# Kernel optimization log

Measured on AMD Instinct MI355X. Metric: run time of the kernel, lower is better.

## Reference

```python
import jax, jax.numpy as jnp
import numpy as np

B, T, W = 8, 4096, 1024          # batch, byte seq len, words per sequence
DB, DW = 64, 512                 # byte_embed_dim, word_embed_dim
NH = 2                           # highway layers per block
VOCAB = 264                      # 256 bytes + 4 + 4 specials
BPE_MARK, WORD_MARK = 4, 3       # bpe_mask_idx, word_mask_idx


def _make_seg_ids():
    # ragged word lengths in {3,4,5}, mean 4, summing to T per sequence
    rng = np.random.default_rng(0)
    seg = np.empty((B, T), np.int32)
    base = T // W
    for b in range(B):
        delta = np.zeros(W, np.int64)
        q = W // 4
        idx = rng.permutation(W)
        delta[idx[:q]] = 1
        delta[idx[q:2 * q]] = -1
        seg[b] = np.repeat(np.arange(W), base + delta)
    return jnp.asarray(seg)


def setup_inputs() -> dict:
    key = jax.random.key(0)
    ks = jax.random.split(key, 12)
    s = 0.05
    byte_tokens = jax.random.randint(ks[0], (B, T), 4, VOCAB)
    bpe_mask = jax.random.bernoulli(ks[1], 0.25, (B, T))
    word_mask = jax.random.bernoulli(ks[2], 0.05, (B, T))
    seg_ids = _make_seg_ids()
    tok_emb = (jax.random.normal(ks[3], (VOCAB, DB)) * s).at[0].set(0.0)  # padding_idx=0 row zeroed
    inp = {
        'byte_tokens': byte_tokens, 'bpe_mask': bpe_mask, 'word_mask': word_mask,
        'seg_ids': seg_ids, 'tok_emb': tok_emb,
        'conv0_w': jax.random.normal(ks[4], (3, DB, DW)) * s, 'conv0_b': jnp.zeros((DW,)),
        'hw0_wg': jax.random.normal(ks[5], (NH, DW, DW)) * s, 'hw0_bg': jnp.zeros((NH, DW)),
        'hw0_wh': jax.random.normal(ks[6], (NH, DW, DW)) * s, 'hw0_bh': jnp.zeros((NH, DW)),
        'conv1_w': jax.random.normal(ks[7], (3, DW, DW)) * s, 'conv1_b': jnp.zeros((DW,)),
        'hw1_wg': jax.random.normal(ks[8], (NH, DW, DW)) * s, 'hw1_bg': jnp.zeros((NH, DW)),
        'hw1_wh': jax.random.normal(ks[9], (NH, DW, DW)) * s, 'hw1_bh': jnp.zeros((NH, DW)),
        'proj_w': jax.random.normal(ks[10], (DW, DW)) * s, 'proj_b': jnp.zeros((DW,)),
    }
    return inp


def _conv_highway(x, cw, cb, wg, bg, wh, bh, residual):
    # 1D same-padded conv over sequence, optional residual, relu, then highways
    y = jax.lax.conv_general_dilated(x, cw, (1,), 'SAME',
                                     dimension_numbers=('NWC', 'WIO', 'NWC')) + cb
    if residual:
        y = y + x
    y = jax.nn.relu(y)
    for i in range(NH):
        g = jax.nn.sigmoid(y @ wg[i] + bg[i])
        h = jax.nn.relu(y @ wh[i] + bh[i])
        y = g * h + (1.0 - g) * y
    return y


def reference(byte_tokens, bpe_mask, word_mask, seg_ids, tok_emb,
              conv0_w, conv0_b, hw0_wg, hw0_bg, hw0_wh, hw0_bh,
              conv1_w, conv1_b, hw1_wg, hw1_bg, hw1_wh, hw1_bh,
              proj_w, proj_b):
    # byte embedding + marker embeddings (pad idx 0 -> zero row)
    x = (tok_emb[byte_tokens]
         + tok_emb[jnp.where(bpe_mask, BPE_MARK, 0)]
         + tok_emb[jnp.where(word_mask, WORD_MARK, 0)])          # [B,T,DB]
    x = _conv_highway(x, conv0_w, conv0_b, hw0_wg, hw0_bg, hw0_wh, hw0_bh, False)
    x = _conv_highway(x, conv1_w, conv1_b, hw1_wg, hw1_bg, hw1_wh, hw1_bh, True)
    # ragged per-word segment max over bytes (fused, replaces python loops)
    seg_max = jax.vmap(lambda xi, si: jax.ops.segment_max(xi, si, num_segments=W))
    x = seg_max(x, seg_ids)                                       # [B,W,DW]
    return x @ proj_w + proj_b
```

## Files before the change

### kernel.cpp

```cpp
#include <hip/hip_runtime.h>
#include <hip/hip_bf16.h>

using bf16 = __hip_bfloat16;
typedef __attribute__((ext_vector_type(8))) short s8v;
typedef __attribute__((ext_vector_type(4))) float f4v;

#define T_SEQ 4096
#define DWC 512

__device__ __forceinline__ float fin(float v) {
    return (v == v && fabsf(v) < 1e30f) ? v : 0.0f;
}
__device__ __forceinline__ float ldf(const void* p, size_t i, int f32) {
    return f32 ? ((const float*)p)[i] : __bfloat162float(((const bf16*)p)[i]);
}
__device__ __forceinline__ float b2f(short s) {
    unsigned u = ((unsigned)(unsigned short)s) << 16;
    return __builtin_bit_cast(float, u);
}
__device__ __forceinline__ short f2b(float v) {
    bf16 b = __float2bfloat16(v);
    return __builtin_bit_cast(short, b);
}
__device__ __forceinline__ uint4 ld16(const short* p) { return *(const uint4*)p; }

__device__ __forceinline__ void swz(int L, int G, int& bx, int& by) {
    int k8 = L & 7, sl = L >> 3;
    int gp = G >> 5;
    bx = sl & 3;
    by = k8 * gp + (sl >> 2);
}

__device__ __forceinline__ int swidx(int row, int ch) {
    return row * 32 + ((ch ^ ((row >> 1) & 3)) << 3);
}

__global__ __launch_bounds__(256) void diag_kernel(bf16* __restrict__ out, int n, float v)
{
    int i = blockIdx.x * 256 + threadIdx.x;
    if (i < n) out[i] = __float2bfloat16(i == 0 ? v : 0.0f);
}

__global__ __launch_bounds__(256) void detect_kernel(
    const int* __restrict__ tok, const unsigned char* __restrict__ bpe,
    const unsigned char* __restrict__ wm, const int* __restrict__ seg,
    const unsigned int* __restrict__ embw, int* __restrict__ flags)
{
    __shared__ int sh[5];
    int tid = threadIdx.x;
    if (tid < 5) sh[tid] = 0;
    __syncthreads();
    int bo = 0, bm = 0, wo = 0, wmid = 0;
    for (int i = tid; i < 16384; i += 256) {
        int odd = 2 * i + 1;
        if (bpe[odd]) bo = 1;
        if (wm[odd])  wo = 1;
        int mid = 8 * (i & 4095) + 4;
        if (bpe[mid]) bm = 1;
        if (wm[mid])  wmid = 1;
    }
    if (bo)   atomicOr(&sh[0], 1);
    if (bm)   atomicOr(&sh[1], 1);
    if (wo)   atomicOr(&sh[2], 1);
    if (wmid) atomicOr(&sh[3], 1);
    if (tid < 32 && embw[32 + tid] != 0u) atomicOr(&sh[4], 1);
    __syncthreads();
    if (tid == 0) {
        flags[0] = (tok[32767] != 0) ? 0 : 1;
        flags[1] = sh[0] ? 1 : (sh[1] ? 4 : 8);
        flags[2] = sh[2] ? 1 : (sh[3] ? 4 : 8);
        flags[3] = (seg[32767] != 0) ? 0 : 1;
        flags[4] = sh[4] ? 0 : 1;
    }
}

#define WB_TOTAL 3249664
__global__ __launch_bounds__(256) void convert_weights(
    const void* c0w, const void* c0b, const void* h0g, const void* h0bg,
    const void* h0h, const void* h0bh, const void* c1w, const void* c1b,
    const void* h1g, const void* h1bg, const void* h1h, const void* h1bh,
    const void* pw, const void* pb, const int* __restrict__ flags,
    short* __restrict__ WB)
{
    int f32 = flags[4];
    size_t i = (size_t)blockIdx.x * 256 + threadIdx.x;
    if (i >= WB_TOTAL) return;
    const void* src; size_t si;
    if (i < 98304)        { size_t n = i / 192, k = i % 192; src = c0w; si = k * 512 + n; }
    else if (i < 98816)   { src = c0b;  si = i - 98304; }
    else if (i < 623104)  { size_t o = i - 98816;  size_t l = o >> 18; o &= 262143;
                            size_t n = o >> 9, k = o & 511; src = h0g; si = (l << 18) + k * 512 + n; }
    else if (i < 624128)  { src = h0bg; si = i - 623104; }
    else if (i < 1148416) { size_t o = i - 624128; size_t l = o >> 18; o &= 262143;
                            size_t n = o >> 9, k = o & 511; src = h0h; si = (l << 18) + k * 512 + n; }
    else if (i < 1149440) { src = h0bh; si = i - 1148416; }
    else if (i < 1935872) { size_t o = i - 1149440; size_t n = o / 1536, k = o % 1536;
                            src = c1w; si = k * 512 + n; }
    else if (i < 1936384) { src = c1b;  si = i - 1935872; }
    else if (i < 2460672) { size_t o = i - 1936384; size_t l = o >> 18; o &= 262143;
                            size_t n = o >> 9, k = o & 511; src = h1g; si = (l << 18) + k * 512 + n; }
    else if (i < 2461696) { src = h1bg; si = i - 2460672; }
    else if (i < 2985984) { size_t o = i - 2461696; size_t l = o >> 18; o &= 262143;
                            size_t n = o >> 9, k = o & 511; src = h1h; si = (l << 18) + k * 512 + n; }
    else if (i < 2987008) { src = h1bh; si = i - 2985984; }
    else if (i < 3249152) { size_t o = i - 2987008; size_t n = o >> 9, k = o & 511;
                            src = pw; si = k * 512 + n; }
    else                  { src = pb;   si = i - 3249152; }
    WB[i] = f2b(ldf(src, si, f32));
}

__global__ __launch_bounds__(256) void embed_kernel(
    const int* __restrict__ tok, const unsigned char* __restrict__ bpe,
    const unsigned char* __restrict__ wm, const void* __restrict__ emb,
    const int* __restrict__ flags, short* __restrict__ xe, int bt0)
{
    int i = blockIdx.x * 256 + threadIdx.x;
    int d = i & 63;
    int btl = i >> 6;
    int bt = bt0 + btl;
    int is64t = flags[0];
    int wb = flags[1], ww = flags[2];
    int f32 = flags[4];
    int t = is64t ? (int)((const long long*)tok)[bt] : tok[bt];
    t = min(max(t, 0), 263);
    float v = ldf(emb, (size_t)t * 64 + d, f32);
    if (bpe[(size_t)bt * wb]) v += ldf(emb, 4 * 64 + d, f32);
    if (wm[(size_t)bt * ww])  v += ldf(emb, 3 * 64 + d, f32);
    xe[i] = f2b(fin(v));
}

template<int IC, bool RESID>
__global__ __launch_bounds__(512) void conv_mfma(
    const short* __restrict__ A, const short* __restrict__ WT,
    const short* __restrict__ bias, short* __restrict__ Out)
{
    constexpr int K = 3 * IC;
    constexpr int NIT = K / 64;
    __shared__ __align__(16) short As[2][256 * 32];
    __shared__ __align__(16) short Bs[2][256 * 32];
    int bx, by;
    swz(blockIdx.x, gridDim.x, bx, by);
    const int bm = by * 128, bn = bx * 128;
    const int tid = threadIdx.x;
    const int wave = tid >> 6, lane = tid & 63;
    const int wmr = (wave >> 1) * 32, wnc = (wave & 1) * 64;
    const int q = lane >> 4, ln16 = lane & 15;
    const int sr = tid >> 2, sch = tid & 3;
    const int tt = (bm + sr) & (T_SEQ - 1);
    const short* Bb = WT + (size_t)(bn + sr) * K + sch * 8;

    f4v acc[2][4] = {};
    uint4 rA0, rA1, rB0, rB1;
    const uint4 z4 = make_uint4(0, 0, 0, 0);

    {
        int ts = tt - 1;
        bool ok = (ts >= 0 && ts < T_SEQ);
        const short* sa = A + (size_t)(bm + sr - 1) * IC + sch * 8;
        rA0 = ok ? ld16(sa) : z4;
        rA1 = ok ? ld16(sa + 32) : z4;
        rB0 = ld16(Bb);
        rB1 = ld16(Bb + 32);
    }
    *(uint4*)(&As[0][swidx(sr, sch)])       = rA0;
    *(uint4*)(&As[0][swidx(128 + sr, sch)]) = rA1;
    *(uint4*)(&Bs[0][swidx(sr, sch)])       = rB0;
    *(uint4*)(&Bs[0][swidx(128 + sr, sch)]) = rB1;
    __syncthreads();
    int p = 0;

    for (int it = 0; it < NIT; ++it) {
        const bool more = (it + 1 < NIT);
        if (more) {
            int kn = (it + 1) * 64;
            int tap = kn / IC, c0 = kn - tap * IC;
            int ts = tt + tap - 1;
            bool ok = (ts >= 0 && ts < T_SEQ);
            const short* sa = A + (size_t)(bm + sr + tap - 1) * IC + c0 + sch * 8;
            rA0 = ok ? ld16(sa) : z4;
            rA1 = ok ? ld16(sa + 32) : z4;
            rB0 = ld16(Bb + kn);
            rB1 = ld16(Bb + kn + 32);
        }
        #pragma unroll
        for (int ks = 0; ks < 2; ks++) {
            s8v af[2], bf[4];
            #pragma unroll
            for (int mi = 0; mi < 2; mi++)
                af[mi] = *(const s8v*)(&As[p][swidx(128 * ks + wmr + mi * 16 + ln16, q)]);
            #pragma unroll
            for (int ni = 0; ni < 4; ni++)
                bf[ni] = *(const s8v*)(&Bs[p][swidx(128 * ks + wnc + ni * 16 + ln16, q)]);
            #pragma unroll
            for (int mi = 0; mi < 2; mi++)
                #pragma unroll
                for (int ni = 0; ni < 4; ni++)
                    acc[mi][ni] = __builtin_amdgcn_mfma_f32_16x16x32_bf16(
                        af[mi], bf[ni], acc[mi][ni], 0, 0, 0);
        }
        if (more) {
            *(uint4*)(&As[p ^ 1][swidx(sr, sch)])       = rA0;
            *(uint4*)(&As[p ^ 1][swidx(128 + sr, sch)]) = rA1;
            *(uint4*)(&Bs[p ^ 1][swidx(sr, sch)])       = rB0;
            *(uint4*)(&Bs[p ^ 1][swidx(128 + sr, sch)]) = rB1;
            __syncthreads();
            p ^= 1;
        }
    }

    #pragma unroll
    for (int mi = 0; mi < 2; mi++)
        #pragma unroll
        for (int ni = 0; ni < 4; ni++) {
            int col = bn + wnc + ni * 16 + ln16;
            float bv = b2f(bias[col]);
            #pragma unroll
            for (int r = 0; r < 4; r++) {
                int orow = bm + wmr + mi * 16 + q * 4 + r;
                float v = acc[mi][ni][r] + bv;
                if constexpr (RESID) v += b2f(A[(size_t)orow * IC + col]);
                Out[(size_t)orow * DWC + col] = f2b(fin(fmaxf(v, 0.0f)));
            }
        }
}

__global__ __launch_bounds__(512) void highway_mfma(
    const short* __restrict__ Y, const short* __restrict__ WgT,
    const short* __restrict__ bg, const short* __restrict__ WhT,
    const short* __restrict__ bh, short* __restrict__ Out)
{
    constexpr int NIT = DWC / 32;
    __shared__ __align__(16) short As[2][128 * 32];
    __shared__ __align__(16) short Bg[2][128 * 32];
    __shared__ __align__(16) short Bh[2][128 * 32];
    int bx, by;
    swz(blockIdx.x, gridDim.x, bx, by);
    const int bm = by * 128, bn = bx * 128;
    const int tid = threadIdx.x;
    const int wave = tid >> 6, lane = tid & 63;
    const int wmr = (wave >> 1) * 32, wnc = (wave & 1) * 64;
    const int q = lane >> 4, ln16 = lane & 15;
    const int sr = tid >> 2, sch = tid & 3;
    const int sw = swidx(sr, sch);
    const short* A0 = Y   + (size_t)(bm + sr) * DWC + sch * 8;
    const short* G0 = WgT + (size_t)(bn + sr) * DWC + sch * 8;
    const short* H0 = WhT + (size_t)(bn + sr) * DWC + sch * 8;

    f4v accg[2][4] = {};
    f4v acch[2][4] = {};
    uint4 rA = ld16(A0), rG = ld16(G0), rH = ld16(H0);
    *(uint4*)(&As[0][sw]) = rA;
    *(uint4*)(&Bg[0][sw]) = rG;
    *(uint4*)(&Bh[0][sw]) = rH;
    __syncthreads();
    int p = 0;

    for (int it = 0; it < NIT; ++it) {
        const bool more = (it + 1 < NIT);
        if (more) {
            int kn = (it + 1) * 32;
            rA = ld16(A0 + kn); rG = ld16(G0 + kn); rH = ld16(H0 + kn);
        }
        s8v af[2], bgf[4], bhf[4];
        #pragma unroll
        for (int mi = 0; mi < 2; mi++) af[mi] = *(const s8v*)(&As[p][swidx(wmr + mi * 16 + ln16, q)]);
        #pragma unroll
        for (int ni = 0; ni < 4; ni++) {
            bgf[ni] = *(const s8v*)(&Bg[p][swidx(wnc + ni * 16 + ln16, q)]);
            bhf[ni] = *(const s8v*)(&Bh[p][swidx(wnc + ni * 16 + ln16, q)]);
        }
        #pragma unroll
        for (int mi = 0; mi < 2; mi++)
            #pragma unroll
            for (int ni = 0; ni < 4; ni++) {
                accg[mi][ni] = __builtin_amdgcn_mfma_f32_16x16x32_bf16(
                    af[mi], bgf[ni], accg[mi][ni], 0, 0, 0);
                acch[mi][ni] = __builtin_amdgcn_mfma_f32_16x16x32_bf16(
                    af[mi], bhf[ni], acch[mi][ni], 0, 0, 0);
            }
        if (more) {
            *(uint4*)(&As[p ^ 1][sw]) = rA;
            *(uint4*)(&Bg[p ^ 1][sw]) = rG;
            *(uint4*)(&Bh[p ^ 1][sw]) = rH;
            __syncthreads();
            p ^= 1;
        }
    }

    #pragma unroll
    for (int mi = 0; mi < 2; mi++)
        #pragma unroll
        for (int ni = 0; ni < 4; ni++) {
            int col = bn + wnc + ni * 16 + ln16;
            float bgv = b2f(bg[col]);
            float bhv = b2f(bh[col]);
            #pragma unroll
            for (int r = 0; r < 4; r++) {
                int orow = bm + wmr + mi * 16 + q * 4 + r;
                float g = 1.0f / (1.0f + expf(-(accg[mi][ni][r] + bgv)));
                float h = fmaxf(acch[mi][ni][r] + bhv, 0.0f);
                float y = b2f(Y[(size_t)orow * DWC + col]);
                Out[(size_t)orow * DWC + col] = f2b(fin(g * h + (1.0f - g) * y));
            }
        }
}

__global__ __launch_bounds__(512) void proj_mfma(
    const short* __restrict__ A, const short* __restrict__ WT,
    const short* __restrict__ bias, const int* __restrict__ flags,
    void* __restrict__ Out, int oroff)
{
    constexpr int NIT = DWC / 32;
    __shared__ __align__(16) short As[2][128 * 32];
    __shared__ __align__(16) short Bs[2][128 * 32];
    int bx, by;
    swz(blockIdx.x, gridDim.x, bx, by);
    const int bm = by * 128, bn = bx * 128;
    const int tid = threadIdx.x;
    const int wave = tid >> 6, lane = tid & 63;
    const int wmr = (wave >> 1) * 32, wnc = (wave & 1) * 64;
    const int q = lane >> 4, ln16 = lane & 15;
    const int sr = tid >> 2, sch = tid & 3;
    const int sw = swidx(sr, sch);
    const int f32 = flags[4];
    const short* A0 = A  + (size_t)(bm + sr) * DWC + sch * 8;
    const short* B0 = WT + (size_t)(bn + sr) * DWC + sch * 8;

    f4v acc[2][4] = {};
    uint4 rA = ld16(A0), rB = ld16(B0);
    *(uint4*)(&As[0][sw]) = rA;
    *(uint4*)(&Bs[0][sw]) = rB;
    __syncthreads();
    int p = 0;

    for (int it = 0; it < NIT; ++it) {
        const bool more = (it + 1 < NIT);
        if (more) {
            int kn = (it + 1) * 32;
            rA = ld16(A0 + kn); rB = ld16(B0 + kn);
        }
        s8v af[2], bf[4];
        #pragma unroll
        for (int mi = 0; mi < 2; mi++) af[mi] = *(const s8v*)(&As[p][swidx(wmr + mi * 16 + ln16, q)]);
        #pragma unroll
        for (int ni = 0; ni < 4; ni++) bf[ni] = *(const s8v*)(&Bs[p][swidx(wnc + ni * 16 + ln16, q)]);
        #pragma unroll
        for (int mi = 0; mi < 2; mi++)
            #pragma unroll
            for (int ni = 0; ni < 4; ni++)
                acc[mi][ni] = __builtin_amdgcn_mfma_f32_16x16x32_bf16(
                    af[mi], bf[ni], acc[mi][ni], 0, 0, 0);
        if (more) {
            *(uint4*)(&As[p ^ 1][sw]) = rA;
            *(uint4*)(&Bs[p ^ 1][sw]) = rB;
            __syncthreads();
            p ^= 1;
        }
    }

    #pragma unroll
    for (int mi = 0; mi < 2; mi++)
        #pragma unroll
        for (int ni = 0; ni < 4; ni++) {
            int col = bn + wnc + ni * 16 + ln16;
            float bv = b2f(bias[col]);
            #pragma unroll
            for (int r = 0; r < 4; r++) {
                int orow = bm + wmr + mi * 16 + q * 4 + r;
                float v = fin(acc[mi][ni][r] + bv);
                size_t oi = (size_t)(oroff + orow) * DWC + col;
                if (f32) ((float*)Out)[oi] = v;
                else     ((bf16*)Out)[oi] = __float2bfloat16(v);
            }
        }
}

__global__ __launch_bounds__(256) void bounds_kernel(
    const int* __restrict__ seg, const int* __restrict__ flags,
    int* __restrict__ wstart, int* __restrict__ wend, int bt0)
{
    int il = blockIdx.x * 256 + threadIdx.x;
    int ig = bt0 + il;
    int is64 = flags[3];
    const long long* seg64 = (const long long*)seg;
    int t = il & (T_SEQ - 1);
    int bl = il >> 12;
    int s  = (is64 ? (int)seg64[ig] : seg[ig]) & 1023;
    int sp = (t == 0)         ? -1 : ((is64 ? (int)seg64[ig - 1] : seg[ig - 1]) & 1023);
    int sn = (t == T_SEQ - 1) ? -1 : ((is64 ? (int)seg64[ig + 1] : seg[ig + 1]) & 1023);
    int bw = (bl << 10) + s;
    if (sp != s) wstart[bw] = t;
    if (sn != s) wend[bw] = t;
}

__global__ __launch_bounds__(512) void segmax_kernel(
    const short* __restrict__ Y, const int* __restrict__ wstart,
    const int* __restrict__ wend, short* __restrict__ Out)
{
    int bw = blockIdx.x;
    int d = threadIdx.x;
    int bl = bw >> 10;
    int s = wstart[bw], e = wend[bw];
    s = min(max(s, 0), T_SEQ - 1);
    e = min(max(e, s), T_SEQ - 1);
    float m = b2f(Y[(size_t)((bl << 12) + s) * DWC + d]);
    for (int t = s + 1; t <= e; ++t)
        m = fmaxf(m, b2f(Y[(size_t)((bl << 12) + t) * DWC + d]));
    Out[(size_t)bw * DWC + d] = f2b(fin(m));
}

extern "C" void kernel_launch(void* const* d_in, const int* in_sizes, int n_in,
                              void* d_out, int out_size, void* d_ws, size_t ws_size,
                              hipStream_t stream)
{
    static const int expect[19] = {32768, 32768, 32768, 32768, 16896,
                                   98304, 512, 524288, 1024, 524288, 1024,
                                   786432, 512, 524288, 1024, 524288, 1024,
                                   262144, 512};
    int bad = -1;
    if (n_in < 19) bad = 31;
    else for (int i = 0; i < 19; i++) if (in_sizes[i] != expect[i]) { bad = i; break; }
    if (bad >= 0) {
        diag_kernel<<<dim3((out_size + 255) / 256), dim3(256), 0, stream>>>(
            (bf16*)d_out, out_size, 1e35f * (float)(1 + bad));
        return;
    }

    char* ws = (char*)d_ws;
    const size_t WBREG = 8ull << 20;
    short* WB    = (short*)ws;
    int*   flags = (int*)(ws + 6500352);
    const size_t perC = 8921088 + 8192 + 64;
    int C = 8;
    while (C > 1 && WBREG + (size_t)C * perC > ws_size) C >>= 1;
    if (WBREG + (size_t)C * perC > ws_size) {
        float ws_mib = (float)((double)ws_size / 1048576.0);
        diag_kernel<<<dim3((out_size + 255) / 256), dim3(256), 0, stream>>>(
            (bf16*)d_out, out_size, 1e30f * (16.0f + ws_mib));
        return;
    }

    const int*  byte_tokens = (const int*)d_in[0];
    const unsigned char* bpe_mask = (const unsigned char*)d_in[1];
    const unsigned char* word_mask = (const unsigned char*)d_in[2];
    const int*  seg_ids     = (const int*)d_in[3];
    const void* tok_emb = d_in[4];

    detect_kernel<<<dim3(1), dim3(256), 0, stream>>>(
        byte_tokens, bpe_mask, word_mask, seg_ids,
        (const unsigned int*)tok_emb, flags);

    convert_weights<<<dim3((WB_TOTAL + 255) / 256), dim3(256), 0, stream>>>(
        d_in[5], d_in[6], d_in[7], d_in[8], d_in[9], d_in[10],
        d_in[11], d_in[12], d_in[13], d_in[14], d_in[15], d_in[16],
        d_in[17], d_in[18], flags, WB);

    short* c0wT = WB;            short* c0b  = WB + 98304;
    short* h0gT = WB + 98816;    short* h0bg = WB + 623104;
    short* h0hT = WB + 624128;   short* h0bh = WB + 1148416;
    short* c1wT = WB + 1149440;  short* c1b  = WB + 1935872;
    short* h1gT = WB + 1936384;  short* h1bg = WB + 2460672;
    short* h1hT = WB + 2461696;  short* h1bh = WB + 2985984;
    short* pwT  = WB + 2987008;  short* pb   = WB + 3249152;
    const int LOFF = 262144, LBOFF = 512;

    for (int b0 = 0; b0 < 8; b0 += C) {
        const int rows  = C * T_SEQ;
        const int words = C * 1024;
        char*  chunk  = ws + WBREG;
        short* xe     = (short*)chunk;
        short* U      = (short*)(chunk + (size_t)C * 524288);
        short* V      = (short*)(chunk + (size_t)C * (524288 + 4194304));
        int*   wstart = (int*)(chunk + (size_t)C * 8912896);
        int*   wend   = wstart + words;
        short* segout = U;

        embed_kernel<<<dim3(rows * 64 / 256), dim3(256), 0, stream>>>(
            byte_tokens, bpe_mask, word_mask, tok_emb, flags, xe, b0 * T_SEQ);

        dim3 gg(4 * (rows / 128));
        conv_mfma<64, false><<<gg, dim3(512), 0, stream>>>(xe, c0wT, c0b, U);

        highway_mfma<<<gg, dim3(512), 0, stream>>>(U, h0gT, h0bg, h0hT, h0bh, V);
        highway_mfma<<<gg, dim3(512), 0, stream>>>(V, h0gT + LOFF, h0bg + LBOFF,
                                                   h0hT + LOFF, h0bh + LBOFF, U);

        conv_mfma<512, true><<<gg, dim3(512), 0, stream>>>(U, c1wT, c1b, V);

        highway_mfma<<<gg, dim3(512), 0, stream>>>(V, h1gT, h1bg, h1hT, h1bh, U);
        highway_mfma<<<gg, dim3(512), 0, stream>>>(U, h1gT + LOFF, h1bg + LBOFF,
                                                   h1hT + LOFF, h1bh + LBOFF, V);

        bounds_kernel<<<dim3(rows / 256), dim3(256), 0, stream>>>(
            seg_ids, flags, wstart, wend, b0 * T_SEQ);

        segmax_kernel<<<dim3(words), dim3(512), 0, stream>>>(V, wstart, wend, segout);

        proj_mfma<<<dim3(4 * (words / 128)), dim3(512), 0, stream>>>(
            segout, pwT, pb, flags, d_out, b0 * 1024);
    }
}
```

Before: 503.7 us.

## Fuse byte embedding into first conv and single-buffer highway/proj LDS tiles

```diff
diff --git a/kernel.cpp b/kernel.cpp
--- a/kernel.cpp
+++ b/kernel.cpp
@@ -75,16 +75,26 @@
 }
 
 #define WB_TOTAL 3249664
+#define EMB4_ELEMS (264 * 4 * 64)
 __global__ __launch_bounds__(256) void convert_weights(
     const void* c0w, const void* c0b, const void* h0g, const void* h0bg,
     const void* h0h, const void* h0bh, const void* c1w, const void* c1b,
     const void* h1g, const void* h1bg, const void* h1h, const void* h1bh,
-    const void* pw, const void* pb, const int* __restrict__ flags,
-    short* __restrict__ WB)
+    const void* pw, const void* pb, const void* emb,
+    const int* __restrict__ flags, short* __restrict__ WB)
 {
     int f32 = flags[4];
     size_t i = (size_t)blockIdx.x * 256 + threadIdx.x;
-    if (i >= WB_TOTAL) return;
+    if (i >= WB_TOTAL + EMB4_ELEMS) return;
+    if (i >= WB_TOTAL) {
+        size_t o = i - WB_TOTAL;
+        size_t t = o >> 8, v = (o >> 6) & 3, c = o & 63;
+        float val = ldf(emb, t * 64 + c, f32);
+        if (v & 1) val += ldf(emb, 4 * 64 + c, f32);
+        if (v & 2) val += ldf(emb, 3 * 64 + c, f32);
+        WB[i] = f2b(fin(val));
+        return;
+    }
     const void* src; size_t si;
     if (i < 98304)        { size_t n = i / 192, k = i % 192; src = c0w; si = k * 512 + n; }
     else if (i < 98816)   { src = c0b;  si = i - 98304; }
@@ -109,31 +119,110 @@
     WB[i] = f2b(ldf(src, si, f32));
 }
 
-__global__ __launch_bounds__(256) void embed_kernel(
+__global__ __launch_bounds__(512) void conv0_mfma(
     const int* __restrict__ tok, const unsigned char* __restrict__ bpe,
-    const unsigned char* __restrict__ wm, const void* __restrict__ emb,
-    const int* __restrict__ flags, short* __restrict__ xe, int bt0)
-{
-    int i = blockIdx.x * 256 + threadIdx.x;
-    int d = i & 63;
-    int btl = i >> 6;
-    int bt = bt0 + btl;
-    int is64t = flags[0];
-    int wb = flags[1], ww = flags[2];
-    int f32 = flags[4];
-    int t = is64t ? (int)((const long long*)tok)[bt] : tok[bt];
-    t = min(max(t, 0), 263);
-    float v = ldf(emb, (size_t)t * 64 + d, f32);
-    if (bpe[(size_t)bt * wb]) v += ldf(emb, 4 * 64 + d, f32);
-    if (wm[(size_t)bt * ww])  v += ldf(emb, 3 * 64 + d, f32);
-    xe[i] = f2b(fin(v));
-}
-
-template<int IC, bool RESID>
-__global__ __launch_bounds__(512) void conv_mfma(
+    const unsigned char* __restrict__ wm, const short* __restrict__ emb4,
+    const int* __restrict__ flags, const short* __restrict__ WT,
+    const short* __restrict__ bias, short* __restrict__ Out)
+{
+    constexpr int K = 192;
+    constexpr int NIT = 3;
+    __shared__ __align__(16) short As[2][256 * 32];
+    __shared__ __align__(16) short Bs[2][256 * 32];
+    int bx, by;
+    swz(blockIdx.x, gridDim.x, bx, by);
+    const int bm = by * 128, bn = bx * 128;
+    const int tid = threadIdx.x;
+    const int wave = tid >> 6, lane = tid & 63;
+    const int wmr = (wave >> 1) * 32, wnc = (wave & 1) * 64;
+    const int q = lane >> 4, ln16 = lane & 15;
+    const int sr = tid >> 2, sch = tid & 3;
+    const int tt = (bm + sr) & (T_SEQ - 1);
+    const int is64t = flags[0];
+    const int wb = flags[1], ww = flags[2];
+    const short* Bb = WT + (size_t)(bn + sr) * K + sch * 8;
+
+    f4v acc[2][4] = {};
+    uint4 rA0, rA1, rB0, rB1;
+    const uint4 z4 = make_uint4(0, 0, 0, 0);
+
+    auto loadA = [&](int tap, uint4& a0, uint4& a1) {
+        int ts = tt + tap - 1;
+        if ((unsigned)ts < (unsigned)T_SEQ) {
+            int bt = bm + sr + tap - 1;
+            int tk = is64t ? (int)((const long long*)tok)[bt] : tok[bt];
+            tk = min(max(tk, 0), 263);
+            int v = (bpe[(size_t)bt * wb] ? 1 : 0) | (wm[(size_t)bt * ww] ? 2 : 0);
+            const short* row = emb4 + ((size_t)tk * 4 + v) * 64;
+            a0 = ld16(row + sch * 8);
+            a1 = ld16(row + 32 + sch * 8);
+        } else { a0 = z4; a1 = z4; }
+    };
+
+    loadA(0, rA0, rA1);
+    rB0 = ld16(Bb);
+    rB1 = ld16(Bb + 32);
+    *(uint4*)(&As[0][swidx(sr, sch)])       = rA0;
+    *(uint4*)(&As[0][swidx(128 + sr, sch)]) = rA1;
+    *(uint4*)(&Bs[0][swidx(sr, sch)])       = rB0;
+    *(uint4*)(&Bs[0][swidx(128 + sr, sch)]) = rB1;
+    __syncthreads();
+    int p = 0;
+
+    for (int it = 0; it < NIT; ++it) {
+        const bool more = (it + 1 < NIT);
+        if (more) {
+            int kn = (it + 1) * 64;
+            loadA(it + 1, rA0, rA1);
+            rB0 = ld16(Bb + kn);
+            rB1 = ld16(Bb + kn + 32);
+        }
+        #pragma unroll
+        for (int ks = 0; ks < 2; ks++) {
+            s8v af[2], bf[4];
+            #pragma unroll
+            for (int mi = 0; mi < 2; mi++)
+                af[mi] = *(const s8v*)(&As[p][swidx(128 * ks + wmr + mi * 16 + ln16, q)]);
+            #pragma unroll
+            for (int ni = 0; ni < 4; ni++)
+                bf[ni] = *(const s8v*)(&Bs[p][swidx(128 * ks + wnc + ni * 16 + ln16, q)]);
+            #pragma unroll
+            for (int mi = 0; mi < 2; mi++)
+                #pragma unroll
+                for (int ni = 0; ni < 4; ni++)
+                    acc[mi][ni] = __builtin_amdgcn_mfma_f32_16x16x32_bf16(
+                        af[mi], bf[ni], acc[mi][ni], 0, 0, 0);
+        }
+        if (more) {
+            *(uint4*)(&As[p ^ 1][swidx(sr, sch)])       = rA0;
+            *(uint4*)(&As[p ^ 1][swidx(128 + sr, sch)]) = rA1;
+            *(uint4*)(&Bs[p ^ 1][swidx(sr, sch)])       = rB0;
+            *(uint4*)(&Bs[p ^ 1][swidx(128 + sr, sch)]) = rB1;
+            __syncthreads();
+            p ^= 1;
+        }
+    }
+
+    #pragma unroll
+    for (int mi = 0; mi < 2; mi++)
+        #pragma unroll
+        for (int ni = 0; ni < 4; ni++) {
+            int col = bn + wnc + ni * 16 + ln16;
+            float bv = b2f(bias[col]);
+            #pragma unroll
+            for (int r = 0; r < 4; r++) {
+                int orow = bm + wmr + mi * 16 + q * 4 + r;
+                Out[(size_t)orow * DWC + col] =
+                    f2b(fin(fmaxf(acc[mi][ni][r] + bv, 0.0f)));
+            }
+        }
+}
+
+__global__ __launch_bounds__(512) void conv1_mfma(
     const short* __restrict__ A, const short* __restrict__ WT,
     const short* __restrict__ bias, short* __restrict__ Out)
 {
+    constexpr int IC = 512;
     constexpr int K = 3 * IC;
     constexpr int NIT = K / 64;
     __shared__ __align__(16) short As[2][256 * 32];
@@ -217,8 +306,7 @@
             #pragma unroll
             for (int r = 0; r < 4; r++) {
                 int orow = bm + wmr + mi * 16 + q * 4 + r;
-                float v = acc[mi][ni][r] + bv;
-                if constexpr (RESID) v += b2f(A[(size_t)orow * IC + col]);
+                float v = acc[mi][ni][r] + bv + b2f(A[(size_t)orow * IC + col]);
                 Out[(size_t)orow * DWC + col] = f2b(fin(fmaxf(v, 0.0f)));
             }
         }
@@ -229,10 +317,9 @@
     const short* __restrict__ bg, const short* __restrict__ WhT,
     const short* __restrict__ bh, short* __restrict__ Out)
 {
-    constexpr int NIT = DWC / 32;
-    __shared__ __align__(16) short As[2][128 * 32];
-    __shared__ __align__(16) short Bg[2][128 * 32];
-    __shared__ __align__(16) short Bh[2][128 * 32];
+    __shared__ __align__(16) short As[128 * 32];
+    __shared__ __align__(16) short Bg[128 * 32];
+    __shared__ __align__(16) short Bh[128 * 32];
     int bx, by;
     swz(blockIdx.x, gridDim.x, bx, by);
     const int bm = by * 128, bn = bx * 128;
@@ -249,25 +336,23 @@
     f4v accg[2][4] = {};
     f4v acch[2][4] = {};
     uint4 rA = ld16(A0), rG = ld16(G0), rH = ld16(H0);
-    *(uint4*)(&As[0][sw]) = rA;
-    *(uint4*)(&Bg[0][sw]) = rG;
-    *(uint4*)(&Bh[0][sw]) = rH;
-    __syncthreads();
-    int p = 0;
-
-    for (int it = 0; it < NIT; ++it) {
-        const bool more = (it + 1 < NIT);
-        if (more) {
-            int kn = (it + 1) * 32;
+
+    for (int k0 = 0; k0 < DWC; k0 += 32) {
+        *(uint4*)(&As[sw]) = rA;
+        *(uint4*)(&Bg[sw]) = rG;
+        *(uint4*)(&Bh[sw]) = rH;
+        __syncthreads();
+        if (k0 + 32 < DWC) {
+            int kn = k0 + 32;
             rA = ld16(A0 + kn); rG = ld16(G0 + kn); rH = ld16(H0 + kn);
         }
         s8v af[2], bgf[4], bhf[4];
         #pragma unroll
-        for (int mi = 0; mi < 2; mi++) af[mi] = *(const s8v*)(&As[p][swidx(wmr + mi * 16 + ln16, q)]);
+        for (int mi = 0; mi < 2; mi++) af[mi] = *(const s8v*)(&As[swidx(wmr + mi * 16 + ln16, q)]);
         #pragma unroll
         for (int ni = 0; ni < 4; ni++) {
-            bgf[ni] = *(const s8v*)(&Bg[p][swidx(wnc + ni * 16 + ln16, q)]);
-            bhf[ni] = *(const s8v*)(&Bh[p][swidx(wnc + ni * 16 + ln16, q)]);
+            bgf[ni] = *(const s8v*)(&Bg[swidx(wnc + ni * 16 + ln16, q)]);
+            bhf[ni] = *(const s8v*)(&Bh[swidx(wnc + ni * 16 + ln16, q)]);
         }
         #pragma unroll
         for (int mi = 0; mi < 2; mi++)
@@ -278,13 +363,7 @@
                 acch[mi][ni] = __builtin_amdgcn_mfma_f32_16x16x32_bf16(
                     af[mi], bhf[ni], acch[mi][ni], 0, 0, 0);
             }
-        if (more) {
-            *(uint4*)(&As[p ^ 1][sw]) = rA;
-            *(uint4*)(&Bg[p ^ 1][sw]) = rG;
-            *(uint4*)(&Bh[p ^ 1][sw]) = rH;
-            __syncthreads();
-            p ^= 1;
-        }
+        __syncthreads();
     }
 
     #pragma unroll
@@ -310,9 +389,8 @@
     const short* __restrict__ bias, const int* __restrict__ flags,
     void* __restrict__ Out, int oroff)
 {
-    constexpr int NIT = DWC / 32;
-    __shared__ __align__(16) short As[2][128 * 32];
-    __shared__ __align__(16) short Bs[2][128 * 32];
+    __shared__ __align__(16) short As[128 * 32];
+    __shared__ __align__(16) short Bs[128 * 32];
     int bx, by;
     swz(blockIdx.x, gridDim.x, bx, by);
     const int bm = by * 128, bn = bx * 128;
@@ -328,34 +406,27 @@
 
     f4v acc[2][4] = {};
     uint4 rA = ld16(A0), rB = ld16(B0);
-    *(uint4*)(&As[0][sw]) = rA;
-    *(uint4*)(&Bs[0][sw]) = rB;
-    __syncthreads();
-    int p = 0;
-
-    for (int it = 0; it < NIT; ++it) {
-        const bool more = (it + 1 < NIT);
-        if (more) {
-            int kn = (it + 1) * 32;
+
+    for (int k0 = 0; k0 < DWC; k0 += 32) {
+        *(uint4*)(&As[sw]) = rA;
+        *(uint4*)(&Bs[sw]) = rB;
+        __syncthreads();
+        if (k0 + 32 < DWC) {
+            int kn = k0 + 32;
             rA = ld16(A0 + kn); rB = ld16(B0 + kn);
         }
         s8v af[2], bf[4];
         #pragma unroll
-        for (int mi = 0; mi < 2; mi++) af[mi] = *(const s8v*)(&As[p][swidx(wmr + mi * 16 + ln16, q)]);
-        #pragma unroll
-        for (int ni = 0; ni < 4; ni++) bf[ni] = *(const s8v*)(&Bs[p][swidx(wnc + ni * 16 + ln16, q)]);
+        for (int mi = 0; mi < 2; mi++) af[mi] = *(const s8v*)(&As[swidx(wmr + mi * 16 + ln16, q)]);
+        #pragma unroll
+        for (int ni = 0; ni < 4; ni++) bf[ni] = *(const s8v*)(&Bs[swidx(wnc + ni * 16 + ln16, q)]);
         #pragma unroll
         for (int mi = 0; mi < 2; mi++)
             #pragma unroll
             for (int ni = 0; ni < 4; ni++)
                 acc[mi][ni] = __builtin_amdgcn_mfma_f32_16x16x32_bf16(
                     af[mi], bf[ni], acc[mi][ni], 0, 0, 0);
-        if (more) {
-            *(uint4*)(&As[p ^ 1][sw]) = rA;
-            *(uint4*)(&Bs[p ^ 1][sw]) = rB;
-            __syncthreads();
-            p ^= 1;
-        }
+        __syncthreads();
     }
 
     #pragma unroll
@@ -429,8 +500,8 @@
     char* ws = (char*)d_ws;
     const size_t WBREG = 8ull << 20;
     short* WB    = (short*)ws;
-    int*   flags = (int*)(ws + 6500352);
-    const size_t perC = 8921088 + 8192 + 64;
+    int*   flags = (int*)(ws + (7u << 20));
+    const size_t perC = 8388608 + 8192 + 64;
     int C = 8;
     while (C > 1 && WBREG + (size_t)C * perC > ws_size) C >>= 1;
     if (WBREG + (size_t)C * perC > ws_size) {
@@ -450,10 +521,10 @@
         byte_tokens, bpe_mask, word_mask, seg_ids,
         (const unsigned int*)tok_emb, flags);
 
-    convert_weights<<<dim3((WB_TOTAL + 255) / 256), dim3(256), 0, stream>>>(
+    convert_weights<<<dim3((WB_TOTAL + EMB4_ELEMS + 255) / 256), dim3(256), 0, stream>>>(
         d_in[5], d_in[6], d_in[7], d_in[8], d_in[9], d_in[10],
         d_in[11], d_in[12], d_in[13], d_in[14], d_in[15], d_in[16],
-        d_in[17], d_in[18], flags, WB);
+        d_in[17], d_in[18], tok_emb, flags, WB);
 
     short* c0wT = WB;            short* c0b  = WB + 98304;
     short* h0gT = WB + 98816;    short* h0bg = WB + 623104;
@@ -462,30 +533,30 @@
     short* h1gT = WB + 1936384;  short* h1bg = WB + 2460672;
     short* h1hT = WB + 2461696;  short* h1bh = WB + 2985984;
     short* pwT  = WB + 2987008;  short* pb   = WB + 3249152;
+    short* emb4 = WB + WB_TOTAL;
     const int LOFF = 262144, LBOFF = 512;
 
     for (int b0 = 0; b0 < 8; b0 += C) {
         const int rows  = C * T_SEQ;
         const int words = C * 1024;
         char*  chunk  = ws + WBREG;
-        short* xe     = (short*)chunk;
-        short* U      = (short*)(chunk + (size_t)C * 524288);
-        short* V      = (short*)(chunk + (size_t)C * (524288 + 4194304));
-        int*   wstart = (int*)(chunk + (size_t)C * 8912896);
+        short* U      = (short*)chunk;
+        short* V      = (short*)(chunk + (size_t)C * 4194304);
+        int*   wstart = (int*)(chunk + (size_t)C * 8388608);
         int*   wend   = wstart + words;
         short* segout = U;
 
-        embed_kernel<<<dim3(rows * 64 / 256), dim3(256), 0, stream>>>(
-            byte_tokens, bpe_mask, word_mask, tok_emb, flags, xe, b0 * T_SEQ);
-
         dim3 gg(4 * (rows / 128));
-        conv_mfma<64, false><<<gg, dim3(512), 0, stream>>>(xe, c0wT, c0b, U);
+        conv0_mfma<<<gg, dim3(512), 0, stream>>>(
+            byte_tokens + (size_t)b0 * T_SEQ,
+            bpe_mask,
+            word_mask, emb4, flags, c0wT, c0b, U);
 
         highway_mfma<<<gg, dim3(512), 0, stream>>>(U, h0gT, h0bg, h0hT, h0bh, V);
         highway_mfma<<<gg, dim3(512), 0, stream>>>(V, h0gT + LOFF, h0bg + LBOFF,
                                                    h0hT + LOFF, h0bh + LBOFF, U);
 
-        conv_mfma<512, true><<<gg, dim3(512), 0, stream>>>(U, c1wT, c1b, V);
+        conv1_mfma<<<gg, dim3(512), 0, stream>>>(U, c1wT, c1b, V);
 
         highway_mfma<<<gg, dim3(512), 0, stream>>>(V, h1gT, h1bg, h1hT, h1bh, U);
         highway_mfma<<<gg, dim3(512), 0, stream>>>(U, h1gT + LOFF, h1bg + LBOFF,
```

Result: faster. 452.0 us (-10.3%).
